# Performance work log

Hardware: AMD Instinct MI355X
Metric: run time of the kernel (lower is better)

Reference implementation:

```python
import jax, jax.numpy as jnp
import numpy as np

F = 64          # in_feature == out_feature
H = 64          # hidden_feature
L = 2           # hidden_layer
B = 32768       # batch


def celu(x):
    # CELU with alpha=1.0: max(0,x) + min(0, exp(x)-1)
    return jnp.where(x > 0, x, jnp.expm1(x))


def setup_inputs() -> dict:
    key = jax.random.key(0)
    ks = jax.random.split(key, 7)
    s_in = 1.0                      # fan_in=1 for first layer
    s_h = 1.0 / np.sqrt(H)
    return {
        "x": jax.random.normal(ks[0], (B, F), dtype=jnp.float32),
        # Linear(1, H) per feature: weight [F, H], bias [F, H]
        "w_in": jax.random.uniform(ks[1], (F, H), jnp.float32, -s_in, s_in),
        "b_in": jax.random.uniform(ks[2], (F, H), jnp.float32, -s_in, s_in),
        # hidden Linear(H, H) per feature per layer: weight [L, F, H(out), H(in)]
        "w_hid": jax.random.uniform(ks[3], (L, F, H, H), jnp.float32, -s_h, s_h),
        "b_hid": jax.random.uniform(ks[4], (L, F, H), jnp.float32, -s_h, s_h),
        # Linear(H, 1) per feature: weight [F, H], bias [F]
        "w_out": jax.random.uniform(ks[5], (F, H), jnp.float32, -s_h, s_h),
        "b_out": jax.random.uniform(ks[6], (F,), jnp.float32, -s_h, s_h),
    }


def reference(x, w_in, b_in, w_hid, b_hid, w_out, b_out):
    # x: [B, F] -> per-feature scalar input to F independent MLPs
    # First layer: Linear(1, H) per feature, then CELU
    h = celu(x[:, :, None] * w_in[None, :, :] + b_in[None, :, :])   # [B, F, H]
    # Hidden layers (small fixed count L) -- batched GEMM over F
    for l in range(L):
        # torch Linear: y = h @ W^T + b, W is [out, in] -> einsum over in-axis
        h = celu(jnp.einsum('bfh,fkh->bfk', h, w_hid[l]) + b_hid[l][None, :, :])
    # Output layer: Linear(H, 1) per feature, concatenated along feature dim
    out = jnp.einsum('bfh,fh->bf', h, w_out) + b_out[None, :]       # [B, F]
    return out
```

## Files before the change

### kernel.cpp

```cpp
#include <hip/hip_runtime.h>

#define F 64
#define H 64
#define NT 256
#define TILE_ROWS 256
#define ITERS 4
#define ROWS_PER_BLOCK (TILE_ROWS * ITERS)
#define WPAD 72

typedef __bf16 bf16;
typedef __attribute__((ext_vector_type(8))) __bf16 bf16x8;
typedef __attribute__((ext_vector_type(4))) __bf16 bf16x4;
typedef __attribute__((ext_vector_type(4))) float f32x4;

__device__ __forceinline__ float celu1(float v) {
    float e = __expf(v) - 1.0f;
    return v > 0.0f ? v : e;
}

__global__ __launch_bounds__(NT, 3) void mlp64(
    const float* __restrict__ x,
    const float* __restrict__ w_in,
    const float* __restrict__ b_in,
    const float* __restrict__ w_hid,
    const float* __restrict__ b_hid,
    const float* __restrict__ w_out,
    const float* __restrict__ b_out,
    float* __restrict__ out,
    int Btot)
{
    const int f    = blockIdx.x & (F - 1);
    const int blk  = blockIdx.x >> 6;
    const int row0 = blk * ROWS_PER_BLOCK;
    const int t    = threadIdx.x;
    const int lane = t & 63;
    const int wave = t >> 6;
    const int l15  = lane & 15;
    const int q    = lane >> 4;
    const int wrow = wave * 64;

    __shared__ __align__(16) bf16 hbuf[TILE_ROWS][WPAD];
    __shared__ __align__(16) bf16 wlds[H][WPAD];
    __shared__ __align__(16) float s_bias[3][H];

    for (int idx = t; idx < 512; idx += NT) {
        const int row = idx >> 3, ch = idx & 7;
        const float* p = w_hid + (((size_t)F + f) << 12) + (row << 6) + (ch << 3);
        float4 a = *(const float4*)p, b = *(const float4*)(p + 4);
        bf16x8 v;
        v[0] = (bf16)a.x; v[1] = (bf16)a.y; v[2] = (bf16)a.z; v[3] = (bf16)a.w;
        v[4] = (bf16)b.x; v[5] = (bf16)b.y; v[6] = (bf16)b.z; v[7] = (bf16)b.w;
        *(bf16x8*)&wlds[row][ch * 8] = v;
    }
    if (t < H)           s_bias[0][t]         = b_in[f * H + t];
    else if (t < 2 * H)  s_bias[1][t - H]     = b_hid[(0 * F + f) * H + (t - H)];
    else if (t < 3 * H)  s_bias[2][t - 2 * H] = b_hid[(1 * F + f) * H + (t - 2 * H)];
    __syncthreads();

    bf16x8 Aw0[4][2];
    #pragma unroll
    for (int m = 0; m < 4; ++m) {
        const float* p = w_hid + ((size_t)f << 12) + (m * 16 + l15) * 64 + q * 8;
        #pragma unroll
        for (int kk = 0; kk < 2; ++kk) {
            float4 a = *(const float4*)(p + kk * 32), b = *(const float4*)(p + kk * 32 + 4);
            bf16x8 v;
            v[0] = (bf16)a.x; v[1] = (bf16)a.y; v[2] = (bf16)a.z; v[3] = (bf16)a.w;
            v[4] = (bf16)b.x; v[5] = (bf16)b.y; v[6] = (bf16)b.z; v[7] = (bf16)b.w;
            Aw0[m][kk] = v;
        }
    }

    bf16x8 A1[4];
    #pragma unroll
    for (int m = 0; m < 4; ++m) {
        float w  = w_in[f * H + m * 16 + l15];
        bf16 hi  = (bf16)w;
        bf16 lo  = (bf16)(w - (float)hi);
        bf16x8 v = {};
        if (q == 0) { v[0] = hi; v[1] = lo; v[2] = hi; }
        A1[m] = v;
    }

    f32x4 wo4[4];
    #pragma unroll
    for (int m = 0; m < 4; ++m)
        wo4[m] = *(const f32x4*)(w_out + f * H + m * 16 + q * 4);
    const float bo = b_out[f];

    float xc[4], xn[4];
    #pragma unroll
    for (int n = 0; n < 4; ++n)
        xc[n] = x[(size_t)(row0 + wrow + n * 16 + l15) * F + f];

    #pragma unroll 1
    for (int it = 0; it < ITERS; ++it) {
        const int rbase = row0 + it * TILE_ROWS + wrow;

        bf16x8 B1[4];
        #pragma unroll
        for (int n = 0; n < 4; ++n) {
            bf16 hh = (bf16)xc[n];
            bf16 ll = (bf16)(xc[n] - (float)hh);
            bf16x8 v = {};
            if (q == 0) { v[0] = hh; v[1] = hh; v[2] = ll; }
            B1[n] = v;
        }
        #pragma unroll
        for (int n = 0; n < 4; ++n)
            xn[n] = (it + 1 < ITERS)
                  ? x[(size_t)(rbase + TILE_ROWS + n * 16 + l15) * F + f] : 0.0f;

        #pragma unroll
        for (int m = 0; m < 4; ++m) {
            f32x4 c0 = *(const f32x4*)&s_bias[0][m * 16 + q * 4];
            f32x4 a[4];
            #pragma unroll
            for (int n = 0; n < 4; ++n)
                a[n] = __builtin_amdgcn_mfma_f32_16x16x32_bf16(A1[m], B1[n], c0, 0, 0, 0);
            #pragma unroll
            for (int n = 0; n < 4; ++n) {
                bf16x4 o;
                #pragma unroll
                for (int rr = 0; rr < 4; ++rr) o[rr] = (bf16)celu1(a[n][rr]);
                *(bf16x4*)&hbuf[wrow + n * 16 + l15][m * 16 + q * 4] = o;
            }
        }

        {
            bf16x8 Bh[4][2];
            #pragma unroll
            for (int n = 0; n < 4; ++n)
                #pragma unroll
                for (int kk = 0; kk < 2; ++kk)
                    Bh[n][kk] = *(const bf16x8*)&hbuf[wrow + n * 16 + l15][kk * 32 + q * 8];
            #pragma unroll
            for (int m = 0; m < 4; ++m) {
                f32x4 c0 = *(const f32x4*)&s_bias[1][m * 16 + q * 4];
                f32x4 a[4];
                #pragma unroll
                for (int n = 0; n < 4; ++n) {
                    a[n] = __builtin_amdgcn_mfma_f32_16x16x32_bf16(Aw0[m][0], Bh[n][0], c0, 0, 0, 0);
                    a[n] = __builtin_amdgcn_mfma_f32_16x16x32_bf16(Aw0[m][1], Bh[n][1], a[n], 0, 0, 0);
                }
                #pragma unroll
                for (int n = 0; n < 4; ++n) {
                    bf16x4 o;
                    #pragma unroll
                    for (int rr = 0; rr < 4; ++rr) o[rr] = (bf16)celu1(a[n][rr]);
                    *(bf16x4*)&hbuf[wrow + n * 16 + l15][m * 16 + q * 4] = o;
                }
            }
        }

        {
            bf16x8 Bh[4][2];
            #pragma unroll
            for (int n = 0; n < 4; ++n)
                #pragma unroll
                for (int kk = 0; kk < 2; ++kk)
                    Bh[n][kk] = *(const bf16x8*)&hbuf[wrow + n * 16 + l15][kk * 32 + q * 8];
            float s[4] = {0.0f, 0.0f, 0.0f, 0.0f};
            #pragma unroll
            for (int m = 0; m < 4; ++m) {
                bf16x8 Awt0 = *(const bf16x8*)&wlds[m * 16 + l15][q * 8];
                bf16x8 Awt1 = *(const bf16x8*)&wlds[m * 16 + l15][32 + q * 8];
                f32x4 c0 = *(const f32x4*)&s_bias[2][m * 16 + q * 4];
                f32x4 a[4];
                #pragma unroll
                for (int n = 0; n < 4; ++n) {
                    a[n] = __builtin_amdgcn_mfma_f32_16x16x32_bf16(Awt0, Bh[n][0], c0, 0, 0, 0);
                    a[n] = __builtin_amdgcn_mfma_f32_16x16x32_bf16(Awt1, Bh[n][1], a[n], 0, 0, 0);
                }
                #pragma unroll
                for (int n = 0; n < 4; ++n)
                    #pragma unroll
                    for (int rr = 0; rr < 4; ++rr)
                        s[n] = fmaf(celu1(a[n][rr]), wo4[m][rr], s[n]);
            }
            #pragma unroll
            for (int n = 0; n < 4; ++n) {
                s[n] += __shfl_xor(s[n], 16, 64);
                s[n] += __shfl_xor(s[n], 32, 64);
            }
            if (q == 0) {
                #pragma unroll
                for (int n = 0; n < 4; ++n)
                    out[(size_t)(rbase + n * 16 + l15) * F + f] = s[n] + bo;
            }
        }

        #pragma unroll
        for (int n = 0; n < 4; ++n) xc[n] = xn[n];
    }
}

extern "C" void kernel_launch(void* const* d_in, const int* in_sizes, int n_in,
                              void* d_out, int out_size, void* d_ws, size_t ws_size,
                              hipStream_t stream) {
    const float* x     = (const float*)d_in[0];
    const float* w_in  = (const float*)d_in[1];
    const float* b_in  = (const float*)d_in[2];
    const float* w_hid = (const float*)d_in[3];
    const float* b_hid = (const float*)d_in[4];
    const float* w_out = (const float*)d_in[5];
    const float* b_out = (const float*)d_in[6];
    float* out = (float*)d_out;

    const int Btot = in_sizes[0] / F;
    dim3 grid((unsigned)((Btot / ROWS_PER_BLOCK) * F));
    dim3 block(NT);
    mlp64<<<grid, block, 0, stream>>>(x, w_in, b_in, w_hid, b_hid, w_out, b_out, out, Btot);
}
```

Measured before the change: 183.8 us.

## Keep hidden activations in registers via 16x16x16 MFMA fragment chaining

Switches from the 16x16x32 bf16 MFMA to the 16x16x16 variant so that each layer's CELU output fragment, held in C/D layout, can be reused directly as the B operand of the next layer. This removes the LDS staging buffer for hidden activations and its write/read round trips. Both hidden weight layers now come from LDS instead of holding one layer in registers, and occupancy is raised to 4 blocks per CU. The cost is twice as many MFMA issues and more per-m LDS weight reads.

Result: slower. 274.5 us (+49.3%).

```diff
diff --git a/kernel.cpp b/kernel.cpp
--- a/kernel.cpp
+++ b/kernel.cpp
@@ -10,7 +10,7 @@
 
 typedef __bf16 bf16;
 typedef __attribute__((ext_vector_type(8))) __bf16 bf16x8;
-typedef __attribute__((ext_vector_type(4))) __bf16 bf16x4;
+typedef __attribute__((ext_vector_type(4))) short s16x4;
 typedef __attribute__((ext_vector_type(4))) float f32x4;
 
 __device__ __forceinline__ float celu1(float v) {
@@ -18,7 +18,23 @@
     return v > 0.0f ? v : e;
 }
 
-__global__ __launch_bounds__(NT, 3) void mlp64(
+__device__ __forceinline__ short bfb(float v) {
+    bf16 h = (bf16)v;
+    return __builtin_bit_cast(short, h);
+}
+
+__device__ __forceinline__ s16x4 celu_frag(f32x4 a) {
+    s16x4 r;
+    r[0] = bfb(celu1(a[0]));
+    r[1] = bfb(celu1(a[1]));
+    r[2] = bfb(celu1(a[2]));
+    r[3] = bfb(celu1(a[3]));
+    return r;
+}
+
+#define MFMA16(A, B, C) __builtin_amdgcn_mfma_f32_16x16x16bf16_1k((A), (B), (C), 0, 0, 0)
+
+__global__ __launch_bounds__(NT, 4) void mlp64(
     const float* __restrict__ x,
     const float* __restrict__ w_in,
     const float* __restrict__ b_in,
@@ -34,50 +50,37 @@
     const int row0 = blk * ROWS_PER_BLOCK;
     const int t    = threadIdx.x;
     const int lane = t & 63;
-    const int wave = t >> 6;
     const int l15  = lane & 15;
     const int q    = lane >> 4;
-    const int wrow = wave * 64;
-
-    __shared__ __align__(16) bf16 hbuf[TILE_ROWS][WPAD];
-    __shared__ __align__(16) bf16 wlds[H][WPAD];
+    const int wrow = (t >> 6) * 64;
+
+    __shared__ __align__(16) bf16  wlds[2][H][WPAD];
     __shared__ __align__(16) float s_bias[3][H];
 
-    for (int idx = t; idx < 512; idx += NT) {
-        const int row = idx >> 3, ch = idx & 7;
-        const float* p = w_hid + (((size_t)F + f) << 12) + (row << 6) + (ch << 3);
+    for (int idx = t; idx < 1024; idx += NT) {
+        const int l   = idx >> 9;
+        const int row = (idx >> 3) & 63;
+        const int ch  = idx & 7;
+        const float* p = w_hid + (((size_t)l * F + f) << 12) + (row << 6) + (ch << 3);
         float4 a = *(const float4*)p, b = *(const float4*)(p + 4);
         bf16x8 v;
         v[0] = (bf16)a.x; v[1] = (bf16)a.y; v[2] = (bf16)a.z; v[3] = (bf16)a.w;
         v[4] = (bf16)b.x; v[5] = (bf16)b.y; v[6] = (bf16)b.z; v[7] = (bf16)b.w;
-        *(bf16x8*)&wlds[row][ch * 8] = v;
+        *(bf16x8*)&wlds[l][row][ch * 8] = v;
     }
     if (t < H)           s_bias[0][t]         = b_in[f * H + t];
     else if (t < 2 * H)  s_bias[1][t - H]     = b_hid[(0 * F + f) * H + (t - H)];
     else if (t < 3 * H)  s_bias[2][t - 2 * H] = b_hid[(1 * F + f) * H + (t - 2 * H)];
     __syncthreads();
 
-    bf16x8 Aw0[4][2];
-    #pragma unroll
-    for (int m = 0; m < 4; ++m) {
-        const float* p = w_hid + ((size_t)f << 12) + (m * 16 + l15) * 64 + q * 8;
-        #pragma unroll
-        for (int kk = 0; kk < 2; ++kk) {
-            float4 a = *(const float4*)(p + kk * 32), b = *(const float4*)(p + kk * 32 + 4);
-            bf16x8 v;
-            v[0] = (bf16)a.x; v[1] = (bf16)a.y; v[2] = (bf16)a.z; v[3] = (bf16)a.w;
-            v[4] = (bf16)b.x; v[5] = (bf16)b.y; v[6] = (bf16)b.z; v[7] = (bf16)b.w;
-            Aw0[m][kk] = v;
-        }
-    }
-
-    bf16x8 A1[4];
+    s16x4 A1[4];
     #pragma unroll
     for (int m = 0; m < 4; ++m) {
         float w  = w_in[f * H + m * 16 + l15];
-        bf16 hi  = (bf16)w;
-        bf16 lo  = (bf16)(w - (float)hi);
-        bf16x8 v = {};
+        bf16 hb  = (bf16)w;
+        short hi = __builtin_bit_cast(short, hb);
+        short lo = bfb(w - (float)hb);
+        s16x4 v  = {};
         if (q == 0) { v[0] = hi; v[1] = lo; v[2] = hi; }
         A1[m] = v;
     }
@@ -97,12 +100,13 @@
     for (int it = 0; it < ITERS; ++it) {
         const int rbase = row0 + it * TILE_ROWS + wrow;
 
-        bf16x8 B1[4];
+        s16x4 B1[4];
         #pragma unroll
         for (int n = 0; n < 4; ++n) {
-            bf16 hh = (bf16)xc[n];
-            bf16 ll = (bf16)(xc[n] - (float)hh);
-            bf16x8 v = {};
+            bf16 hb  = (bf16)xc[n];
+            short hh = __builtin_bit_cast(short, hb);
+            short ll = bfb(xc[n] - (float)hb);
+            s16x4 v  = {};
             if (q == 0) { v[0] = hh; v[1] = hh; v[2] = ll; }
             B1[n] = v;
         }
@@ -111,66 +115,58 @@
             xn[n] = (it + 1 < ITERS)
                   ? x[(size_t)(rbase + TILE_ROWS + n * 16 + l15) * F + f] : 0.0f;
 
+        s16x4 Bh[4][4];
         #pragma unroll
         for (int m = 0; m < 4; ++m) {
             f32x4 c0 = *(const f32x4*)&s_bias[0][m * 16 + q * 4];
             f32x4 a[4];
             #pragma unroll
             for (int n = 0; n < 4; ++n)
-                a[n] = __builtin_amdgcn_mfma_f32_16x16x32_bf16(A1[m], B1[n], c0, 0, 0, 0);
+                a[n] = MFMA16(A1[m], B1[n], c0);
+            #pragma unroll
+            for (int n = 0; n < 4; ++n)
+                Bh[n][m] = celu_frag(a[n]);
+        }
+
+        s16x4 Bh2[4][4];
+        #pragma unroll
+        for (int m = 0; m < 4; ++m) {
+            s16x4 Aw[4];
+            #pragma unroll
+            for (int kf = 0; kf < 4; ++kf)
+                Aw[kf] = *(const s16x4*)&wlds[0][m * 16 + l15][kf * 16 + q * 4];
+            f32x4 c0 = *(const f32x4*)&s_bias[1][m * 16 + q * 4];
+            f32x4 a[4];
             #pragma unroll
             for (int n = 0; n < 4; ++n) {
-                bf16x4 o;
-                #pragma unroll
-                for (int rr = 0; rr < 4; ++rr) o[rr] = (bf16)celu1(a[n][rr]);
-                *(bf16x4*)&hbuf[wrow + n * 16 + l15][m * 16 + q * 4] = o;
-            }
+                f32x4 acc = MFMA16(Aw[0], Bh[n][0], c0);
+                acc = MFMA16(Aw[1], Bh[n][1], acc);
+                acc = MFMA16(Aw[2], Bh[n][2], acc);
+                acc = MFMA16(Aw[3], Bh[n][3], acc);
+                a[n] = acc;
+            }
+            #pragma unroll
+            for (int n = 0; n < 4; ++n)
+                Bh2[n][m] = celu_frag(a[n]);
         }
 
         {
-            bf16x8 Bh[4][2];
-            #pragma unroll
-            for (int n = 0; n < 4; ++n)
-                #pragma unroll
-                for (int kk = 0; kk < 2; ++kk)
-                    Bh[n][kk] = *(const bf16x8*)&hbuf[wrow + n * 16 + l15][kk * 32 + q * 8];
+            float s[4] = {0.0f, 0.0f, 0.0f, 0.0f};
             #pragma unroll
             for (int m = 0; m < 4; ++m) {
-                f32x4 c0 = *(const f32x4*)&s_bias[1][m * 16 + q * 4];
-                f32x4 a[4];
-                #pragma unroll
-                for (int n = 0; n < 4; ++n) {
-                    a[n] = __builtin_amdgcn_mfma_f32_16x16x32_bf16(Aw0[m][0], Bh[n][0], c0, 0, 0, 0);
-                    a[n] = __builtin_amdgcn_mfma_f32_16x16x32_bf16(Aw0[m][1], Bh[n][1], a[n], 0, 0, 0);
-                }
-                #pragma unroll
-                for (int n = 0; n < 4; ++n) {
-                    bf16x4 o;
-                    #pragma unroll
-                    for (int rr = 0; rr < 4; ++rr) o[rr] = (bf16)celu1(a[n][rr]);
-                    *(bf16x4*)&hbuf[wrow + n * 16 + l15][m * 16 + q * 4] = o;
-                }
-            }
-        }
-
-        {
-            bf16x8 Bh[4][2];
-            #pragma unroll
-            for (int n = 0; n < 4; ++n)
-                #pragma unroll
-                for (int kk = 0; kk < 2; ++kk)
-                    Bh[n][kk] = *(const bf16x8*)&hbuf[wrow + n * 16 + l15][kk * 32 + q * 8];
-            float s[4] = {0.0f, 0.0f, 0.0f, 0.0f};
-            #pragma unroll
-            for (int m = 0; m < 4; ++m) {
-                bf16x8 Awt0 = *(const bf16x8*)&wlds[m * 16 + l15][q * 8];
-                bf16x8 Awt1 = *(const bf16x8*)&wlds[m * 16 + l15][32 + q * 8];
+                s16x4 Aw[4];
+                #pragma unroll
+                for (int kf = 0; kf < 4; ++kf)
+                    Aw[kf] = *(const s16x4*)&wlds[1][m * 16 + l15][kf * 16 + q * 4];
                 f32x4 c0 = *(const f32x4*)&s_bias[2][m * 16 + q * 4];
                 f32x4 a[4];
                 #pragma unroll
                 for (int n = 0; n < 4; ++n) {
-                    a[n] = __builtin_amdgcn_mfma_f32_16x16x32_bf16(Awt0, Bh[n][0], c0, 0, 0, 0);
-                    a[n] = __builtin_amdgcn_mfma_f32_16x16x32_bf16(Awt1, Bh[n][1], a[n], 0, 0, 0);
+                    f32x4 acc = MFMA16(Aw[0], Bh2[n][0], c0);
+                    acc = MFMA16(Aw[1], Bh2[n][1], acc);
+                    acc = MFMA16(Aw[2], Bh2[n][2], acc);
+                    acc = MFMA16(Aw[3], Bh2[n][3], acc);
+                    a[n] = acc;
                 }
                 #pragma unroll
                 for (int n = 0; n < 4; ++n)
```
